# Optimization experiments

Measured on AMD Instinct MI355X. Metric: run time of the kernel, lower is better.

Reference implementation:

```python
import jax, jax.numpy as jnp
import numpy as np

B, S, HID = 1, 2048, 2048
NH, NKV = 16, 4
HD = HID // NH  # 128


def _rope_manual(x, cos_h, sin_h):
    # x: [B, S, nh, HD]; cos_h/sin_h: [1, S, 1, HD//2]
    d = x.shape[-1]
    x_rot = x[..., : d // 2]
    x_pass = x[..., d // 2:]
    # rotate interleaved pairs inside the first half
    x_rot = jnp.stack([-x_rot[..., 1::2], x_rot[..., ::2]], axis=-1)
    x_rot = x_rot.reshape(x_rot.shape[:-2] + (d // 2,))
    return jnp.concatenate(
        [x_rot * cos_h + x_pass * sin_h, -x_rot * sin_h + x_pass * cos_h], axis=-1
    )


def setup_inputs() -> dict:
    key = jax.random.key(0)
    ks = jax.random.split(key, 7)
    bound = 1.0 / np.sqrt(HID)
    return {
        "x": jax.random.normal(ks[0], (B, S, HID), jnp.float32),
        "cos": jax.random.uniform(ks[1], (S, HD), jnp.float32),
        "sin": jax.random.uniform(ks[2], (S, HD), jnp.float32),
        "wq": jax.random.uniform(ks[3], (NH * HD, HID), jnp.float32, -bound, bound),
        "wk": jax.random.uniform(ks[4], (NKV * HD, HID), jnp.float32, -bound, bound),
        "wv": jax.random.uniform(ks[5], (NKV * HD, HID), jnp.float32, -bound, bound),
        "wo": jax.random.uniform(ks[6], (HID, HID), jnp.float32, -bound, bound),
    }


def reference(x, cos, sin, wq, wk, wv, wo):
    b, s, _ = x.shape
    q = jnp.einsum("bsh,oh->bso", x, wq).reshape(b, s, NH, HD)
    k = jnp.einsum("bsh,oh->bso", x, wk).reshape(b, s, NKV, HD)
    v = jnp.einsum("bsh,oh->bso", x, wv).reshape(b, s, NKV, HD)

    cos_h = cos[None, :, None, : HD // 2]  # [1,S,1,HD/2]
    sin_h = sin[None, :, None, : HD // 2]
    q = _rope_manual(q, cos_h, sin_h)
    k = _rope_manual(k, cos_h, sin_h)

    # [B, H, S, D]
    q = q.transpose(0, 2, 1, 3)
    k = k.transpose(0, 2, 1, 3)
    v = v.transpose(0, 2, 1, 3)
    # GQA kv repeat (repeat_interleave over head dim)
    rep = NH // NKV
    k = jnp.repeat(k, rep, axis=1)
    v = jnp.repeat(v, rep, axis=1)

    scale = 1.0 / np.sqrt(HD).astype(np.float32)
    scores = jnp.einsum("bhqd,bhkd->bhqk", q, k) * scale
    causal = jnp.tril(jnp.ones((s, s), bool))
    scores = jnp.where(causal[None, None], scores, jnp.finfo(scores.dtype).min)
    attn = jax.nn.softmax(scores, axis=-1)
    out = jnp.einsum("bhqk,bhkd->bhqd", attn, v)  # [B,H,S,D]
    out = out.transpose(0, 2, 1, 3).reshape(b, s, NH * HD)
    return jnp.einsum("bso,ho->bsh", out, wo)
```

## Files before the change

kernel.cpp:

```cpp
#include <hip/hip_runtime.h>
#include <hip/hip_bf16.h>

typedef __bf16 bf16_t;
typedef __attribute__((ext_vector_type(8))) __bf16 bf16x8;
typedef __attribute__((ext_vector_type(4))) __bf16 bf16x4;
typedef __attribute__((ext_vector_type(4))) float f32x4;

#define S_LEN 2048
#define HID 2048
#define NH 16
#define NKV 4
#define HD 128

__device__ __forceinline__ void gll16(const bf16_t* g, bf16_t* l) {
    __builtin_amdgcn_global_load_lds(
        (const __attribute__((address_space(1))) unsigned int*)g,
        (__attribute__((address_space(3))) unsigned int*)l, 16, 0, 0);
}

__device__ __forceinline__ bf16x8 cvt2x4(float4 a, float4 b) {
    bf16x8 o;
    o[0]=(bf16_t)a.x; o[1]=(bf16_t)a.y; o[2]=(bf16_t)a.z; o[3]=(bf16_t)a.w;
    o[4]=(bf16_t)b.x; o[5]=(bf16_t)b.y; o[6]=(bf16_t)b.z; o[7]=(bf16_t)b.w;
    return o;
}

__global__ __launch_bounds__(256) void cvt_all(
    const float* __restrict__ x,  const float* __restrict__ wq,
    const float* __restrict__ wk, const float* __restrict__ wv,
    bf16_t* __restrict__ xb, bf16_t* __restrict__ wb)
{
    const size_t M = 1024 * 1024;
    size_t g = ((size_t)blockIdx.x * 256 + threadIdx.x) * 8;
    const float* src; bf16_t* dst; size_t soff, doff;
    if (g < 4 * M) {
        src = x; dst = xb; soff = g; doff = g;
    } else {
        size_t w = g - 4 * M; dst = wb; doff = w;
        if (w < 4 * M)      { src = wq; soff = w; }
        else if (w < 5 * M) { src = wk; soff = w - 4 * M; }
        else                { src = wv; soff = w - 5 * M; }
    }
    float4 a = *(const float4*)&src[soff];
    float4 b = *(const float4*)&src[soff + 4];
    *(bf16x8*)&dst[doff] = cvt2x4(a, b);
}

__global__ __launch_bounds__(256) void cvt_f32_bf16(const float* __restrict__ in,
                                                    bf16_t* __restrict__ out, int n)
{
    int i = (blockIdx.x * 256 + threadIdx.x) * 8;
    if (i >= n) return;
    float4 a = *(const float4*)&in[i];
    float4 b = *(const float4*)&in[i + 4];
    *(bf16x8*)&out[i] = cvt2x4(a, b);
}

template<int MODE, typename CT>
__global__ __launch_bounds__(256, 4) void gemm128x64(
    const bf16_t* __restrict__ A, const bf16_t* __restrict__ B,
    CT* __restrict__ C, bf16_t* __restrict__ CkP, bf16_t* __restrict__ CvtP,
    int N, int K)
{
    __shared__ __align__(16) bf16_t sA[2][128 * 64];
    __shared__ __align__(16) bf16_t sB[2][64 * 64];

    const int tid = threadIdx.x, lane = tid & 63, wave = tid >> 6;
    const int l16 = lane & 15, quad = lane >> 4;
    const int m0 = blockIdx.y * 128, n0 = blockIdx.x * 64;
    const int wm = (wave >> 1) * 64, wn = (wave & 1) * 32;

    const bf16_t* gA[4]; const bf16_t* gB[2];
    int laOff[4], lbOff[2];
#pragma unroll
    for (int t = 0; t < 4; t++) {
        int p = (wave * 4 + t) * 64 + lane;
        int row = p >> 3;
        int lc = (p & 7) ^ (row & 7);
        gA[t] = A + (size_t)(m0 + row) * K + lc * 8;
        laOff[t] = (wave * 4 + t) * 512;
    }
#pragma unroll
    for (int t = 0; t < 2; t++) {
        int p = (wave * 2 + t) * 64 + lane;
        int row = p >> 3;
        int lc = (p & 7) ^ (row & 7);
        gB[t] = B + (size_t)(n0 + row) * K + lc * 8;
        lbOff[t] = (wave * 2 + t) * 512;
    }

    int offA[2][4], offB[2][2];
#pragma unroll
    for (int kc = 0; kc < 2; kc++) {
#pragma unroll
        for (int i = 0; i < 4; i++) {
            int rm = wm + i * 16 + l16;
            offA[kc][i] = rm * 64 + (((kc * 4 + quad) ^ (rm & 7)) * 8);
        }
#pragma unroll
        for (int j = 0; j < 2; j++) {
            int rn = wn + j * 16 + l16;
            offB[kc][j] = rn * 64 + (((kc * 4 + quad) ^ (rn & 7)) * 8);
        }
    }

    f32x4 acc[4][2] = {};

#pragma unroll
    for (int t = 0; t < 4; t++) { gll16(gA[t], &sA[0][laOff[t]]); gA[t] += 64; }
#pragma unroll
    for (int t = 0; t < 2; t++) { gll16(gB[t], &sB[0][lbOff[t]]); gB[t] += 64; }
    __syncthreads();

    int bsel = 0;
    for (int k0 = 0; k0 < K; k0 += 64) {
        const int ns = bsel ^ 1;
        if (k0 + 64 < K) {
#pragma unroll
            for (int t = 0; t < 4; t++) { gll16(gA[t], &sA[ns][laOff[t]]); gA[t] += 64; }
#pragma unroll
            for (int t = 0; t < 2; t++) { gll16(gB[t], &sB[ns][lbOff[t]]); gB[t] += 64; }
        }

#pragma unroll
        for (int kc = 0; kc < 2; kc++) {
            bf16x8 af[4], bfv[2];
#pragma unroll
            for (int i = 0; i < 4; i++) af[i] = *(bf16x8*)&sA[bsel][offA[kc][i]];
#pragma unroll
            for (int j = 0; j < 2; j++) bfv[j] = *(bf16x8*)&sB[bsel][offB[kc][j]];
#pragma unroll
            for (int i = 0; i < 4; i++)
#pragma unroll
                for (int j = 0; j < 2; j++)
                    acc[i][j] = __builtin_amdgcn_mfma_f32_16x16x32_bf16(af[i], bfv[j], acc[i][j], 0, 0, 0);
        }

        __syncthreads();
        bsel = ns;
    }

#pragma unroll
    for (int i = 0; i < 4; i++) {
        int rowb = m0 + wm + i * 16 + quad * 4;
#pragma unroll
        for (int j = 0; j < 2; j++) {
            int col = n0 + wn + j * 16 + l16;
#pragma unroll
            for (int r = 0; r < 4; r++) {
                float v = acc[i][j][r];
                int row = rowb + r;
                if (MODE == 0) {
                    C[(size_t)row * N + col] = (CT)v;
                } else {
                    if (col < 2048)      C[(size_t)row * 2048 + col] = (CT)v;
                    else if (col < 2560) CkP[(size_t)row * 512 + (col - 2048)] = (bf16_t)v;
                    else                 CvtP[(size_t)(col - 2560) * S_LEN + row] = (bf16_t)v;
                }
            }
        }
    }
}

__global__ void rope_all(bf16_t* __restrict__ Qh, bf16_t* __restrict__ Kh,
                         const float* __restrict__ cosb, const float* __restrict__ sinb)
{
    int s = blockIdx.x;
    int grp = blockIdx.y;
    int sub = threadIdx.x >> 5;
    int i = threadIdx.x & 31;
    bf16_t* row = (grp < 4) ? (Qh + ((size_t)s * NH + grp * 4 + sub) * HD)
                            : (Kh + ((size_t)s * NKV + sub) * HD);
    float x0 = (float)row[2 * i];
    float x1 = (float)row[2 * i + 1];
    float p0 = (float)row[64 + 2 * i];
    float p1 = (float)row[64 + 2 * i + 1];
    float c0 = cosb[s * HD + 2 * i];
    float c1 = cosb[s * HD + 2 * i + 1];
    float n0 = sinb[s * HD + 2 * i];
    float n1 = sinb[s * HD + 2 * i + 1];
    float r0 = -x1, r1 = x0;
    row[2 * i]          = (bf16_t)(r0 * c0 + p0 * n0);
    row[2 * i + 1]      = (bf16_t)(r1 * c1 + p1 * n1);
    row[64 + 2 * i]     = (bf16_t)(-r0 * n0 + p0 * c0);
    row[64 + 2 * i + 1] = (bf16_t)(-r1 * n1 + p1 * c1);
}

__global__ __launch_bounds__(512, 1) void flash_attn10(
    const bf16_t* __restrict__ Q,
    const bf16_t* __restrict__ Kb,
    const bf16_t* __restrict__ VT,
    bf16_t* __restrict__ OpD,
    bf16_t* __restrict__ OpX,
    float* __restrict__ lpart,
    int S)
{
    __shared__ __align__(16) bf16_t sK[2][64 * 136];
    __shared__ __align__(16) bf16_t sVT[2][128 * 72];
    __shared__ __align__(16) bf16_t sP[8][16 * 72];

    const int c   = blockIdx.x;
    const int kvh = blockIdx.y;
    const int p   = c >> 2, sub = c & 3;
    const int ts   = (33 * sub + 3) >> 2;
    const int tend = (33 * sub + 36) >> 2;
    const int tA   = p + 1;

    const int tid = threadIdx.x, lane = tid & 63, wave = tid >> 6;
    const int l16 = lane & 15, quad = lane >> 4;
    const int rowg = wave & 3;
    const int h0   = kvh * 4 + (wave >> 2) * 2;
    const float scale = 0.08838834764831845f;

    int krow[2], kcol[2], vrow[2], vcol[2];
#pragma unroll
    for (int it = 0; it < 2; it++) {
        int cc = tid + 512 * it;
        krow[it] = cc >> 4; kcol[it] = (cc & 15) * 8;
        vrow[it] = cc >> 3; vcol[it] = (cc & 7) * 8;
    }

#pragma unroll
    for (int sI = 0; sI < 2; sI++) {
        int st0, st1, sqt, ssl;
        if (sI == 0) {
            if (ts < tA) { st0 = ts; st1 = (tend < tA ? tend : tA); sqt = p;      ssl = c; }
            else         { st0 = ts; st1 = tend;                    sqt = 31 - p; ssl = c; }
        } else {
            if (!(ts < tA && tend > tA)) break;
            st0 = tA; st1 = tend; sqt = 31 - p; ssl = 64 + p;
        }
        const int base = (sqt == p) ? 0 : tA;
        const int kb = st0 - base, ke = st1 - base;
        const int qt = sqt;
        const int q0 = qt * 64;
        const int qrow = q0 + rowg * 16 + l16;

        bf16x8 qf[2][4];
#pragma unroll
        for (int h = 0; h < 2; h++)
#pragma unroll
            for (int cc = 0; cc < 4; cc++)
                qf[h][cc] = *(const bf16x8*)&Q[(size_t)qrow * HID + (h0 + h) * HD + cc * 32 + quad * 8];

        f32x4 oacc[2][8] = {};
        float lsum[2] = {0.f, 0.f};

        bf16x8 kpre[2], vpre[2];
#pragma unroll
        for (int it = 0; it < 2; it++) {
            kpre[it] = *(const bf16x8*)&Kb[(size_t)(kb * 64 + krow[it]) * (NKV * HD) + kvh * HD + kcol[it]];
            vpre[it] = *(const bf16x8*)&VT[((size_t)kvh * HD + vrow[it]) * S + kb * 64 + vcol[it]];
        }
#pragma unroll
        for (int it = 0; it < 2; it++) {
            *(bf16x8*)&sK[0][krow[it] * 136 + kcol[it]] = kpre[it];
            *(bf16x8*)&sVT[0][vrow[it] * 72 + vcol[it]] = vpre[it];
        }
        if (kb + 1 < ke) {
            const int t1 = (kb + 1) * 64;
#pragma unroll
            for (int it = 0; it < 2; it++) {
                kpre[it] = *(const bf16x8*)&Kb[(size_t)(t1 + krow[it]) * (NKV * HD) + kvh * HD + kcol[it]];
                vpre[it] = *(const bf16x8*)&VT[((size_t)kvh * HD + vrow[it]) * S + t1 + vcol[it]];
            }
        }
        __syncthreads();

        int sel = 0;
        for (int kt = kb; kt < ke; kt++) {
            const int t0 = kt * 64;
            const int ns = sel ^ 1;

            if (kt + 1 < ke) {
#pragma unroll
                for (int it = 0; it < 2; it++) {
                    *(bf16x8*)&sK[ns][krow[it] * 136 + kcol[it]] = kpre[it];
                    *(bf16x8*)&sVT[ns][vrow[it] * 72 + vcol[it]] = vpre[it];
                }
                if (kt + 2 < ke) {
                    const int t2 = t0 + 128;
#pragma unroll
                    for (int it = 0; it < 2; it++) {
                        kpre[it] = *(const bf16x8*)&Kb[(size_t)(t2 + krow[it]) * (NKV * HD) + kvh * HD + kcol[it]];
                        vpre[it] = *(const bf16x8*)&VT[((size_t)kvh * HD + vrow[it]) * S + t2 + vcol[it]];
                    }
                }
            }

            f32x4 sc[2][4];
            __builtin_amdgcn_s_setprio(1);
#pragma unroll
            for (int nt = 0; nt < 4; nt++) {
                bf16x8 kf[4];
#pragma unroll
                for (int cc = 0; cc < 4; cc++)
                    kf[cc] = *(bf16x8*)&sK[sel][(nt * 16 + l16) * 136 + cc * 32 + quad * 8];
#pragma unroll
                for (int h = 0; h < 2; h++) {
                    f32x4 d = {};
#pragma unroll
                    for (int cc = 0; cc < 4; cc++)
                        d = __builtin_amdgcn_mfma_f32_16x16x32_bf16(kf[cc], qf[h][cc], d, 0, 0, 0);
                    sc[h][nt] = d;
                }
            }
            __builtin_amdgcn_s_setprio(0);

            bf16x8 pa[2][2];
            if (kt == qt) {
#pragma unroll
                for (int h = 0; h < 2; h++) {
#pragma unroll
                    for (int nt = 0; nt < 4; nt++) {
                        const int tbk = t0 + nt * 16 + quad * 4;
                        bf16x4 pk;
#pragma unroll
                        for (int r = 0; r < 4; r++) {
                            float pv = (tbk + r <= qrow) ? __expf(sc[h][nt][r] * scale) : 0.0f;
                            lsum[h] += pv;
                            pk[r] = (bf16_t)pv;
                        }
                        *(bf16x4*)&sP[wave][l16 * 72 + nt * 16 + quad * 4] = pk;
                    }
#pragma unroll
                    for (int kc = 0; kc < 2; kc++)
                        pa[h][kc] = *(bf16x8*)&sP[wave][l16 * 72 + kc * 32 + quad * 8];
                }
            } else {
#pragma unroll
                for (int h = 0; h < 2; h++) {
#pragma unroll
                    for (int nt = 0; nt < 4; nt++) {
                        bf16x4 pk;
#pragma unroll
                        for (int r = 0; r < 4; r++) {
                            float pv = __expf(sc[h][nt][r] * scale);
                            lsum[h] += pv;
                            pk[r] = (bf16_t)pv;
                        }
                        *(bf16x4*)&sP[wave][l16 * 72 + nt * 16 + quad * 4] = pk;
                    }
#pragma unroll
                    for (int kc = 0; kc < 2; kc++)
                        pa[h][kc] = *(bf16x8*)&sP[wave][l16 * 72 + kc * 32 + quad * 8];
                }
            }

            __builtin_amdgcn_s_setprio(1);
#pragma unroll
            for (int dt = 0; dt < 8; dt++)
#pragma unroll
                for (int kc = 0; kc < 2; kc++) {
                    bf16x8 vf = *(bf16x8*)&sVT[sel][(dt * 16 + l16) * 72 + kc * 32 + quad * 8];
#pragma unroll
                    for (int h = 0; h < 2; h++)
                        oacc[h][dt] = __builtin_amdgcn_mfma_f32_16x16x32_bf16(pa[h][kc], vf, oacc[h][dt], 0, 0, 0);
                }
            __builtin_amdgcn_s_setprio(0);

            __syncthreads();
            sel = ns;
        }

        const int sg = kvh * 80 + ssl;
        bf16_t* Op = (sg < 256) ? (OpD + (size_t)sg * 32768)
                                : (OpX + (size_t)(sg - 256) * 32768);
#pragma unroll
        for (int h = 0; h < 2; h++) {
            const int hl = (wave >> 2) * 2 + h;
            float lr = lsum[h];
            lr += __shfl_xor(lr, 16, 64);
            lr += __shfl_xor(lr, 32, 64);
            if (quad == 0)
                lpart[(size_t)sg * 256 + (rowg * 16 + l16) * 4 + hl] = lr;
#pragma unroll
            for (int r = 0; r < 4; r++) {
                int rr = rowg * 16 + quad * 4 + r;
#pragma unroll
                for (int dt = 0; dt < 8; dt++)
                    Op[((size_t)rr * 4 + hl) * 128 + dt * 16 + l16] =
                        (bf16_t)(oacc[h][dt][r]);
            }
        }
    }
}

__global__ __launch_bounds__(256) void flash_combine10(
    const bf16_t* __restrict__ OpD, const bf16_t* __restrict__ OpX,
    const float* __restrict__ lpart, bf16_t* __restrict__ oh)
{
    int i = (blockIdx.x * 256 + threadIdx.x) * 8;
    int s = i >> 11;
    int h = (i >> 7) & 15;
    int col = i & 127;
    int qt = s >> 6;
    int base80 = (h >> 2) * 80;
    int roff = (s & 63) * 4 + (h & 3);

    int sl[4]; int nsl = 0;
    if (qt <= 15) {
        int pr = qt;
#pragma unroll
        for (int sub = 0; sub < 4; sub++) {
            int tss = (33 * sub + 3) >> 2;
            if (tss < qt + 1) sl[nsl++] = pr * 4 + sub;
        }
    } else {
        int pr = 31 - qt, tAh = pr + 1;
#pragma unroll
        for (int sub = 0; sub < 4; sub++) {
            int tss = (33 * sub + 3) >> 2;
            int ten = (33 * sub + 36) >> 2;
            if (ten > tAh) sl[nsl++] = (tss < tAh) ? 64 + pr : pr * 4 + sub;
        }
    }

    float acc[8] = {0.f, 0.f, 0.f, 0.f, 0.f, 0.f, 0.f, 0.f};
    float l = 0.f;
    for (int ci = 0; ci < nsl; ci++) {
        int sg = base80 + sl[ci];
        const bf16_t* P = (sg < 256) ? (OpD + (size_t)sg * 32768)
                                     : (OpX + (size_t)(sg - 256) * 32768);
        bf16x8 a = *(const bf16x8*)&P[(size_t)roff * 128 + col];
#pragma unroll
        for (int j = 0; j < 8; j++) acc[j] += (float)a[j];
        l += lpart[(size_t)sg * 256 + roff];
    }
    float inv = 1.0f / l;
    bf16x8 o;
#pragma unroll
    for (int j = 0; j < 8; j++)
        o[j] = (bf16_t)(acc[j] * inv);
    *(bf16x8*)&oh[i] = o;
}

extern "C" void kernel_launch(void* const* d_in, const int* in_sizes, int n_in,
                              void* d_out, int out_size, void* d_ws, size_t ws_size,
                              hipStream_t stream)
{
    const float* x    = (const float*)d_in[0];
    const float* cosb = (const float*)d_in[1];
    const float* sinb = (const float*)d_in[2];
    const float* wq   = (const float*)d_in[3];
    const float* wk   = (const float*)d_in[4];
    const float* wv   = (const float*)d_in[5];
    const float* wo   = (const float*)d_in[6];
    float* out = (float*)d_out;

    char* ws = (char*)d_ws;
    bf16_t* wb = (bf16_t*)(ws);
    bf16_t* qh = (bf16_t*)(ws + (size_t)12 * 1024 * 1024);
    bf16_t* kh = (bf16_t*)(ws + (size_t)20 * 1024 * 1024);
    bf16_t* vT = (bf16_t*)(ws + (size_t)22 * 1024 * 1024);
    float*  lp = (float*) (ws + (size_t)24 * 1024 * 1024);
    bf16_t* opx = (bf16_t*)(ws + (size_t)24 * 1024 * 1024 + 512 * 1024);
    bf16_t* xb  = (bf16_t*)d_out;
    bf16_t* opd = (bf16_t*)d_out;

    const int NX = S_LEN * HID;

    cvt_all<<<10 * 1024 * 1024 / (256 * 8), 256, 0, stream>>>(
        x, wq, wk, wv, xb, wb);

    gemm128x64<1, bf16_t><<<dim3(48, 16), 256, 0, stream>>>(xb, wb, qh, kh, vT, 3072, HID);

    rope_all<<<dim3(S_LEN, 5), 128, 0, stream>>>(qh, kh, cosb, sinb);

    cvt_f32_bf16<<<NX / (256 * 8), 256, 0, stream>>>(wo, wb, NX);

    flash_attn10<<<dim3(64, NKV), 512, 0, stream>>>(qh, kh, vT, opd, opx, lp, S_LEN);

    flash_combine10<<<NX / (256 * 8), 256, 0, stream>>>(opd, opx, lp, qh);

    gemm128x64<0, float><<<dim3(32, 16), 256, 0, stream>>>(qh, wb, out, nullptr, nullptr, HID, HID);
}
```

Before: 212.9 us.

## Process all four GQA heads per wave in attention and fold wo conversion into cvt_all

The attention kernel moves from 8 waves (each owning 2 heads of a 16-row slice) to 4 waves, each owning all 4 query heads sharing the KV head. Each K/V fragment read from shared memory now feeds twice as many MFMAs, and there are fewer waves per block. The cost is double the accumulator and score registers per wave and half the waves available to hide latency. Separately, the wo fp32-to-bf16 conversion moves into the single cvt_all launch, writing to a new workspace region, which removes one kernel launch.

```diff
diff --git a/kernel.cpp b/kernel.cpp
--- a/kernel.cpp
+++ b/kernel.cpp
@@ -28,32 +28,25 @@
 __global__ __launch_bounds__(256) void cvt_all(
     const float* __restrict__ x,  const float* __restrict__ wq,
     const float* __restrict__ wk, const float* __restrict__ wv,
-    bf16_t* __restrict__ xb, bf16_t* __restrict__ wb)
+    const float* __restrict__ wo, bf16_t* __restrict__ xb,
+    bf16_t* __restrict__ wb, bf16_t* __restrict__ wob)
 {
     const size_t M = 1024 * 1024;
     size_t g = ((size_t)blockIdx.x * 256 + threadIdx.x) * 8;
     const float* src; bf16_t* dst; size_t soff, doff;
     if (g < 4 * M) {
         src = x; dst = xb; soff = g; doff = g;
-    } else {
+    } else if (g < 10 * M) {
         size_t w = g - 4 * M; dst = wb; doff = w;
         if (w < 4 * M)      { src = wq; soff = w; }
         else if (w < 5 * M) { src = wk; soff = w - 4 * M; }
         else                { src = wv; soff = w - 5 * M; }
+    } else {
+        src = wo; dst = wob; soff = g - 10 * M; doff = soff;
     }
     float4 a = *(const float4*)&src[soff];
     float4 b = *(const float4*)&src[soff + 4];
     *(bf16x8*)&dst[doff] = cvt2x4(a, b);
-}
-
-__global__ __launch_bounds__(256) void cvt_f32_bf16(const float* __restrict__ in,
-                                                    bf16_t* __restrict__ out, int n)
-{
-    int i = (blockIdx.x * 256 + threadIdx.x) * 8;
-    if (i >= n) return;
-    float4 a = *(const float4*)&in[i];
-    float4 b = *(const float4*)&in[i + 4];
-    *(bf16x8*)&out[i] = cvt2x4(a, b);
 }
 
 template<int MODE, typename CT>
@@ -186,7 +179,7 @@
     row[64 + 2 * i + 1] = (bf16_t)(-r1 * n1 + p1 * c1);
 }
 
-__global__ __launch_bounds__(512, 1) void flash_attn10(
+__global__ __launch_bounds__(256, 1) void flash_attn11(
     const bf16_t* __restrict__ Q,
     const bf16_t* __restrict__ Kb,
     const bf16_t* __restrict__ VT,
@@ -197,7 +190,7 @@
 {
     __shared__ __align__(16) bf16_t sK[2][64 * 136];
     __shared__ __align__(16) bf16_t sVT[2][128 * 72];
-    __shared__ __align__(16) bf16_t sP[8][16 * 72];
+    __shared__ __align__(16) bf16_t sP[4][16 * 72];
 
     const int c   = blockIdx.x;
     const int kvh = blockIdx.y;
@@ -208,14 +201,14 @@
 
     const int tid = threadIdx.x, lane = tid & 63, wave = tid >> 6;
     const int l16 = lane & 15, quad = lane >> 4;
-    const int rowg = wave & 3;
-    const int h0   = kvh * 4 + (wave >> 2) * 2;
+    const int rowg = wave;
+    const int h0   = kvh * 4;
     const float scale = 0.08838834764831845f;
 
-    int krow[2], kcol[2], vrow[2], vcol[2];
-#pragma unroll
-    for (int it = 0; it < 2; it++) {
-        int cc = tid + 512 * it;
+    int krow[4], kcol[4], vrow[4], vcol[4];
+#pragma unroll
+    for (int it = 0; it < 4; it++) {
+        int cc = tid + 256 * it;
         krow[it] = cc >> 4; kcol[it] = (cc & 15) * 8;
         vrow[it] = cc >> 3; vcol[it] = (cc & 7) * 8;
     }
@@ -236,31 +229,31 @@
         const int q0 = qt * 64;
         const int qrow = q0 + rowg * 16 + l16;
 
-        bf16x8 qf[2][4];
-#pragma unroll
-        for (int h = 0; h < 2; h++)
+        bf16x8 qf[4][4];
+#pragma unroll
+        for (int h = 0; h < 4; h++)
 #pragma unroll
             for (int cc = 0; cc < 4; cc++)
                 qf[h][cc] = *(const bf16x8*)&Q[(size_t)qrow * HID + (h0 + h) * HD + cc * 32 + quad * 8];
 
-        f32x4 oacc[2][8] = {};
-        float lsum[2] = {0.f, 0.f};
-
-        bf16x8 kpre[2], vpre[2];
-#pragma unroll
-        for (int it = 0; it < 2; it++) {
+        f32x4 oacc[4][8] = {};
+        float lsum[4] = {0.f, 0.f, 0.f, 0.f};
+
+        bf16x8 kpre[4], vpre[4];
+#pragma unroll
+        for (int it = 0; it < 4; it++) {
             kpre[it] = *(const bf16x8*)&Kb[(size_t)(kb * 64 + krow[it]) * (NKV * HD) + kvh * HD + kcol[it]];
             vpre[it] = *(const bf16x8*)&VT[((size_t)kvh * HD + vrow[it]) * S + kb * 64 + vcol[it]];
         }
 #pragma unroll
-        for (int it = 0; it < 2; it++) {
+        for (int it = 0; it < 4; it++) {
             *(bf16x8*)&sK[0][krow[it] * 136 + kcol[it]] = kpre[it];
             *(bf16x8*)&sVT[0][vrow[it] * 72 + vcol[it]] = vpre[it];
         }
         if (kb + 1 < ke) {
             const int t1 = (kb + 1) * 64;
 #pragma unroll
-            for (int it = 0; it < 2; it++) {
+            for (int it = 0; it < 4; it++) {
                 kpre[it] = *(const bf16x8*)&Kb[(size_t)(t1 + krow[it]) * (NKV * HD) + kvh * HD + kcol[it]];
                 vpre[it] = *(const bf16x8*)&VT[((size_t)kvh * HD + vrow[it]) * S + t1 + vcol[it]];
             }
@@ -274,21 +267,21 @@
 
             if (kt + 1 < ke) {
 #pragma unroll
-                for (int it = 0; it < 2; it++) {
+                for (int it = 0; it < 4; it++) {
                     *(bf16x8*)&sK[ns][krow[it] * 136 + kcol[it]] = kpre[it];
                     *(bf16x8*)&sVT[ns][vrow[it] * 72 + vcol[it]] = vpre[it];
                 }
                 if (kt + 2 < ke) {
                     const int t2 = t0 + 128;
 #pragma unroll
-                    for (int it = 0; it < 2; it++) {
+                    for (int it = 0; it < 4; it++) {
                         kpre[it] = *(const bf16x8*)&Kb[(size_t)(t2 + krow[it]) * (NKV * HD) + kvh * HD + kcol[it]];
                         vpre[it] = *(const bf16x8*)&VT[((size_t)kvh * HD + vrow[it]) * S + t2 + vcol[it]];
                     }
                 }
             }
 
-            f32x4 sc[2][4];
+            f32x4 sc[4][4];
             __builtin_amdgcn_s_setprio(1);
 #pragma unroll
             for (int nt = 0; nt < 4; nt++) {
@@ -297,7 +290,7 @@
                 for (int cc = 0; cc < 4; cc++)
                     kf[cc] = *(bf16x8*)&sK[sel][(nt * 16 + l16) * 136 + cc * 32 + quad * 8];
 #pragma unroll
-                for (int h = 0; h < 2; h++) {
+                for (int h = 0; h < 4; h++) {
                     f32x4 d = {};
 #pragma unroll
                     for (int cc = 0; cc < 4; cc++)
@@ -307,10 +300,10 @@
             }
             __builtin_amdgcn_s_setprio(0);
 
-            bf16x8 pa[2][2];
+            bf16x8 pa[4][2];
             if (kt == qt) {
 #pragma unroll
-                for (int h = 0; h < 2; h++) {
+                for (int h = 0; h < 4; h++) {
 #pragma unroll
                     for (int nt = 0; nt < 4; nt++) {
                         const int tbk = t0 + nt * 16 + quad * 4;
@@ -329,7 +322,7 @@
                 }
             } else {
 #pragma unroll
-                for (int h = 0; h < 2; h++) {
+                for (int h = 0; h < 4; h++) {
 #pragma unroll
                     for (int nt = 0; nt < 4; nt++) {
                         bf16x4 pk;
@@ -354,7 +347,7 @@
                 for (int kc = 0; kc < 2; kc++) {
                     bf16x8 vf = *(bf16x8*)&sVT[sel][(dt * 16 + l16) * 72 + kc * 32 + quad * 8];
 #pragma unroll
-                    for (int h = 0; h < 2; h++)
+                    for (int h = 0; h < 4; h++)
                         oacc[h][dt] = __builtin_amdgcn_mfma_f32_16x16x32_bf16(pa[h][kc], vf, oacc[h][dt], 0, 0, 0);
                 }
             __builtin_amdgcn_s_setprio(0);
@@ -367,19 +360,18 @@
         bf16_t* Op = (sg < 256) ? (OpD + (size_t)sg * 32768)
                                 : (OpX + (size_t)(sg - 256) * 32768);
 #pragma unroll
-        for (int h = 0; h < 2; h++) {
-            const int hl = (wave >> 2) * 2 + h;
+        for (int h = 0; h < 4; h++) {
             float lr = lsum[h];
             lr += __shfl_xor(lr, 16, 64);
             lr += __shfl_xor(lr, 32, 64);
             if (quad == 0)
-                lpart[(size_t)sg * 256 + (rowg * 16 + l16) * 4 + hl] = lr;
+                lpart[(size_t)sg * 256 + (rowg * 16 + l16) * 4 + h] = lr;
 #pragma unroll
             for (int r = 0; r < 4; r++) {
                 int rr = rowg * 16 + quad * 4 + r;
 #pragma unroll
                 for (int dt = 0; dt < 8; dt++)
-                    Op[((size_t)rr * 4 + hl) * 128 + dt * 16 + l16] =
+                    Op[((size_t)rr * 4 + h) * 128 + dt * 16 + l16] =
                         (bf16_t)(oacc[h][dt][r]);
             }
         }
@@ -455,23 +447,22 @@
     bf16_t* vT = (bf16_t*)(ws + (size_t)22 * 1024 * 1024);
     float*  lp = (float*) (ws + (size_t)24 * 1024 * 1024);
     bf16_t* opx = (bf16_t*)(ws + (size_t)24 * 1024 * 1024 + 512 * 1024);
+    bf16_t* wob = (bf16_t*)(ws + (size_t)28 * 1024 * 1024 + 512 * 1024);
     bf16_t* xb  = (bf16_t*)d_out;
     bf16_t* opd = (bf16_t*)d_out;
 
     const int NX = S_LEN * HID;
 
-    cvt_all<<<10 * 1024 * 1024 / (256 * 8), 256, 0, stream>>>(
-        x, wq, wk, wv, xb, wb);
+    cvt_all<<<14 * 1024 * 1024 / (256 * 8), 256, 0, stream>>>(
+        x, wq, wk, wv, wo, xb, wb, wob);
 
     gemm128x64<1, bf16_t><<<dim3(48, 16), 256, 0, stream>>>(xb, wb, qh, kh, vT, 3072, HID);
 
     rope_all<<<dim3(S_LEN, 5), 128, 0, stream>>>(qh, kh, cosb, sinb);
 
-    cvt_f32_bf16<<<NX / (256 * 8), 256, 0, stream>>>(wo, wb, NX);
-
-    flash_attn10<<<dim3(64, NKV), 512, 0, stream>>>(qh, kh, vT, opd, opx, lp, S_LEN);
+    flash_attn11<<<dim3(64, NKV), 256, 0, stream>>>(qh, kh, vT, opd, opx, lp, S_LEN);
 
     flash_combine10<<<NX / (256 * 8), 256, 0, stream>>>(opd, opx, lp, qh);
 
-    gemm128x64<0, float><<<dim3(32, 16), 256, 0, stream>>>(qh, wb, out, nullptr, nullptr, HID, HID);
-}
+    gemm128x64<0, float><<<dim3(32, 16), 256, 0, stream>>>(qh, wob, out, nullptr, nullptr, HID, HID);
+}
```

After: 212.9 us. No clear change (-0.0%).
